# Performance work log

Hardware: AMD Instinct MI355X
Metric: run time of the kernel (lower is better)

Reference implementation:

```python
import jax, jax.numpy as jnp
import numpy as np

DIM = 512
RANK = 256
ORDER = 4
BATCH = 100000
INIT_STD = 0.01


def setup_inputs() -> dict:
    key = jax.random.key(0)
    ks = jax.random.split(key, ORDER + 1)
    inp = {}
    for i in range(ORDER):
        inp[f"f{i}"] = jax.random.normal(ks[i], (DIM, RANK), dtype=jnp.float32) * INIT_STD
    inp["tensor_of_indices"] = jax.random.randint(ks[ORDER], (BATCH, ORDER), 0, DIM, dtype=jnp.int64)
    return inp


def reference(f0, f1, f2, f3, tensor_of_indices):
    # value[b] = sum_r prod_i factors[i][idx[b, i], r]
    # (same math as reconstructing the full CP tensor and gathering entries,
    #  but computed directly per queried index)
    factors = (f0, f1, f2, f3)
    # gather factor rows per mode: each [B, rank]
    prod = factors[0][tensor_of_indices[:, 0]]
    for i in range(1, ORDER):
        prod = prod * factors[i][tensor_of_indices[:, i]]
    return jnp.sum(prod, axis=-1)  # [B]
```

## Files before the change

kernel.cpp:

```cpp
#include <hip/hip_runtime.h>


#define RANK 256

__global__ __launch_bounds__(256) void cp_gather_kernel(
    const float* __restrict__ f0, const float* __restrict__ f1,
    const float* __restrict__ f2, const float* __restrict__ f3,
    const int*   __restrict__ idx,
    float*       __restrict__ out, int batch)
{
    const int wave = (int)((blockIdx.x * blockDim.x + threadIdx.x) >> 6);
    const int lane = (int)(threadIdx.x & 63);
    if (wave >= batch) return;

    const int4 iv = *reinterpret_cast<const int4*>(idx + wave * 4);

    const int r = lane * 4;
    const float4 a = *reinterpret_cast<const float4*>(f0 + (size_t)iv.x * RANK + r);
    const float4 b = *reinterpret_cast<const float4*>(f1 + (size_t)iv.y * RANK + r);
    const float4 c = *reinterpret_cast<const float4*>(f2 + (size_t)iv.z * RANK + r);
    const float4 d = *reinterpret_cast<const float4*>(f3 + (size_t)iv.w * RANK + r);

    float s = a.x * b.x * c.x * d.x
            + a.y * b.y * c.y * d.y
            + a.z * b.z * c.z * d.z
            + a.w * b.w * c.w * d.w;

    #pragma unroll
    for (int off = 32; off > 0; off >>= 1)
        s += __shfl_down(s, off);

    if (lane == 0) out[wave] = s;
}

extern "C" void kernel_launch(void* const* d_in, const int* in_sizes, int n_in,
                              void* d_out, int out_size, void* d_ws, size_t ws_size,
                              hipStream_t stream) {
    const float* f0  = (const float*)d_in[0];
    const float* f1  = (const float*)d_in[1];
    const float* f2  = (const float*)d_in[2];
    const float* f3  = (const float*)d_in[3];
    const int*   idx = (const int*)d_in[4];
    float* out = (float*)d_out;

    const int batch = out_size;
    const int threads = 256;
    const int waves_per_block = threads / 64;
    const int grid = (batch + waves_per_block - 1) / waves_per_block;

    cp_gather_kernel<<<grid, threads, 0, stream>>>(f0, f1, f2, f3, idx, out, batch);
}
```

Measured before the change: 21.72 us.

## Convert factor matrices to fp16 in workspace and gather multiple entries per wave

Adds a pre-pass that converts the four fp32 factor matrices to fp16 in the workspace. A new gather kernel then reads half-width rows and splits each wave into two 32-lane halves, with each wave handling 8 batch entries. The aim is to halve gathered bytes and spread per-wave index-load and reduction overhead over more entries. It adds an extra kernel launch and conversion pass each call, and loses precision by rounding the factors to fp16. An fp32 fallback that processes 4 entries per wave is kept for when the workspace is too small.

After: 20.43 us. 1.06x faster.

```diff
diff --git a/kernel.cpp b/kernel.cpp
--- a/kernel.cpp
+++ b/kernel.cpp
@@ -1,36 +1,134 @@
 #include <hip/hip_runtime.h>
+#include <hip/hip_fp16.h>
 
 
-#define RANK 256
+#define RANK   256
+#define FELEMS (512 * 256)
+#define EPW    8
 
-__global__ __launch_bounds__(256) void cp_gather_kernel(
+__global__ __launch_bounds__(256) void cp_convert_f16(
+    const float* __restrict__ f0, const float* __restrict__ f1,
+    const float* __restrict__ f2, const float* __restrict__ f3,
+    __half* __restrict__ ws)
+{
+    const float* srcs[4] = {f0, f1, f2, f3};
+    const float* __restrict__ src = srcs[blockIdx.y];
+    __half* __restrict__ dst = ws + (size_t)blockIdx.y * FELEMS;
+
+    const int base = (blockIdx.x * 256 + threadIdx.x) * 8;
+    if (base >= FELEMS) return;
+
+    const float4 a = *reinterpret_cast<const float4*>(src + base);
+    const float4 b = *reinterpret_cast<const float4*>(src + base + 4);
+    union { uint4 u; __half2 h[4]; } pk;
+    pk.h[0] = __float22half2_rn(make_float2(a.x, a.y));
+    pk.h[1] = __float22half2_rn(make_float2(a.z, a.w));
+    pk.h[2] = __float22half2_rn(make_float2(b.x, b.y));
+    pk.h[3] = __float22half2_rn(make_float2(b.z, b.w));
+    *reinterpret_cast<uint4*>(dst + base) = pk.u;
+}
+
+__device__ __forceinline__ void cvt8(const uint4 u, float* v) {
+    const __half2* h = reinterpret_cast<const __half2*>(&u);
+    float2 t;
+    t = __half22float2(h[0]); v[0] = t.x; v[1] = t.y;
+    t = __half22float2(h[1]); v[2] = t.x; v[3] = t.y;
+    t = __half22float2(h[2]); v[4] = t.x; v[5] = t.y;
+    t = __half22float2(h[3]); v[6] = t.x; v[7] = t.y;
+}
+
+__global__ __launch_bounds__(256) void cp_gather_f16(
+    const __half* __restrict__ ws, const int* __restrict__ idx,
+    float* __restrict__ out, int batch)
+{
+    const int wid  = (int)((blockIdx.x * blockDim.x + threadIdx.x) >> 6);
+    const int lane = (int)(threadIdx.x & 63);
+    const int e0   = wid * EPW;
+    if (e0 >= batch) return;
+
+    const int half_id = lane >> 5;
+    const int l5      = lane & 31;
+    const int r0      = l5 * 8;
+
+    int  ee[4];
+    int4 iv[4];
+    #pragma unroll
+    for (int p = 0; p < 4; ++p) {
+        ee[p] = e0 + 2 * p + half_id;
+        const int ec = ee[p] < batch ? ee[p] : batch - 1;
+        iv[p] = *reinterpret_cast<const int4*>(idx + (size_t)ec * 4);
+    }
+
+    uint4 raw[4][4];
+    #pragma unroll
+    for (int p = 0; p < 4; ++p) {
+        raw[p][0] = *reinterpret_cast<const uint4*>(ws + 0 * FELEMS + (size_t)iv[p].x * RANK + r0);
+        raw[p][1] = *reinterpret_cast<const uint4*>(ws + 1 * FELEMS + (size_t)iv[p].y * RANK + r0);
+        raw[p][2] = *reinterpret_cast<const uint4*>(ws + 2 * FELEMS + (size_t)iv[p].z * RANK + r0);
+        raw[p][3] = *reinterpret_cast<const uint4*>(ws + 3 * FELEMS + (size_t)iv[p].w * RANK + r0);
+    }
+
+    float s[4];
+    #pragma unroll
+    for (int p = 0; p < 4; ++p) {
+        float va[8], vb[8], vc[8], vd[8];
+        cvt8(raw[p][0], va);
+        cvt8(raw[p][1], vb);
+        cvt8(raw[p][2], vc);
+        cvt8(raw[p][3], vd);
+        float acc = 0.f;
+        #pragma unroll
+        for (int k = 0; k < 8; ++k)
+            acc += va[k] * vb[k] * vc[k] * vd[k];
+        s[p] = acc;
+    }
+
+    #pragma unroll
+    for (int off = 16; off > 0; off >>= 1) {
+        #pragma unroll
+        for (int p = 0; p < 4; ++p)
+            s[p] += __shfl_xor(s[p], off);
+    }
+
+    if (l5 == 0) {
+        #pragma unroll
+        for (int p = 0; p < 4; ++p)
+            if (ee[p] < batch) out[ee[p]] = s[p];
+    }
+}
+
+__global__ __launch_bounds__(256) void cp_gather_f32(
     const float* __restrict__ f0, const float* __restrict__ f1,
     const float* __restrict__ f2, const float* __restrict__ f3,
     const int*   __restrict__ idx,
     float*       __restrict__ out, int batch)
 {
-    const int wave = (int)((blockIdx.x * blockDim.x + threadIdx.x) >> 6);
+    const int wid  = (int)((blockIdx.x * blockDim.x + threadIdx.x) >> 6);
     const int lane = (int)(threadIdx.x & 63);
-    if (wave >= batch) return;
-
-    const int4 iv = *reinterpret_cast<const int4*>(idx + wave * 4);
-
+    const int e0   = wid * 4;
+    if (e0 >= batch) return;
     const int r = lane * 4;
-    const float4 a = *reinterpret_cast<const float4*>(f0 + (size_t)iv.x * RANK + r);
-    const float4 b = *reinterpret_cast<const float4*>(f1 + (size_t)iv.y * RANK + r);
-    const float4 c = *reinterpret_cast<const float4*>(f2 + (size_t)iv.z * RANK + r);
-    const float4 d = *reinterpret_cast<const float4*>(f3 + (size_t)iv.w * RANK + r);
-
-    float s = a.x * b.x * c.x * d.x
-            + a.y * b.y * c.y * d.y
-            + a.z * b.z * c.z * d.z
-            + a.w * b.w * c.w * d.w;
-
+    float s[4];
+    #pragma unroll
+    for (int e = 0; e < 4; ++e) {
+        const int  ec = (e0 + e) < batch ? (e0 + e) : batch - 1;
+        const int4 iv = *reinterpret_cast<const int4*>(idx + (size_t)ec * 4);
+        const float4 a = *reinterpret_cast<const float4*>(f0 + (size_t)iv.x * RANK + r);
+        const float4 b = *reinterpret_cast<const float4*>(f1 + (size_t)iv.y * RANK + r);
+        const float4 c = *reinterpret_cast<const float4*>(f2 + (size_t)iv.z * RANK + r);
+        const float4 d = *reinterpret_cast<const float4*>(f3 + (size_t)iv.w * RANK + r);
+        s[e] = a.x * b.x * c.x * d.x + a.y * b.y * c.y * d.y
+             + a.z * b.z * c.z * d.z + a.w * b.w * c.w * d.w;
+    }
     #pragma unroll
     for (int off = 32; off > 0; off >>= 1)
-        s += __shfl_down(s, off);
-
-    if (lane == 0) out[wave] = s;
+        #pragma unroll
+        for (int e = 0; e < 4; ++e)
+            s[e] += __shfl_xor(s[e], off);
+    if (lane == 0)
+        #pragma unroll
+        for (int e = 0; e < 4; ++e)
+            if (e0 + e < batch) out[e0 + e] = s[e];
 }
 
 extern "C" void kernel_launch(void* const* d_in, const int* in_sizes, int n_in,
@@ -42,11 +140,18 @@
     const float* f3  = (const float*)d_in[3];
     const int*   idx = (const int*)d_in[4];
     float* out = (float*)d_out;
+    const int batch = out_size;
 
-    const int batch = out_size;
-    const int threads = 256;
-    const int waves_per_block = threads / 64;
-    const int grid = (batch + waves_per_block - 1) / waves_per_block;
-
-    cp_gather_kernel<<<grid, threads, 0, stream>>>(f0, f1, f2, f3, idx, out, batch);
+    const size_t ws_needed = (size_t)4 * FELEMS * sizeof(__half);
+    if (ws_size >= ws_needed) {
+        __half* wsf = (__half*)d_ws;
+        dim3 cgrid(FELEMS / (256 * 8), 4);
+        cp_convert_f16<<<cgrid, 256, 0, stream>>>(f0, f1, f2, f3, wsf);
+        const int waves = (batch + EPW - 1) / EPW;
+        const int grid  = (waves + 3) / 4;
+        cp_gather_f16<<<grid, 256, 0, stream>>>(wsf, idx, out, batch);
+    } else {
+        const int grid = (batch + 15) / 16;
+        cp_gather_f32<<<grid, 256, 0, stream>>>(f0, f1, f2, f3, idx, out, batch);
+    }
 }
```

## Stage fp16 rank-sliced factor tiles in LDS with split-rank partial sums

Applied to the files above, without the earlier changes.

Adds a three-kernel path. The first kernel converts the factor matrices to fp16 and lays them out in rank slices of 16. The main kernel then loads one slice of all four factors into 64 KB of swizzled LDS, and each thread computes a partial dot product for its batch elements from that slice. A third kernel sums the 16 partials per element. The aim is to replace scattered global gathers with LDS reads, at the cost of fp16 precision loss, two extra launches and partial-sum traffic through global memory.

Result: slower. 24.45 us (+12.6%).

```diff
diff --git a/kernel.cpp b/kernel.cpp
--- a/kernel.cpp
+++ b/kernel.cpp
@@ -1,36 +1,136 @@
 #include <hip/hip_runtime.h>
+#include <hip/hip_fp16.h>
 
 
-#define RANK 256
+#define DIM    512
+#define RANK   256
+#define W      16
+#define NS     16
+#define NCHUNK 32
+#define FELEMS (DIM * RANK)
 
-__global__ __launch_bounds__(256) void cp_gather_kernel(
+__global__ __launch_bounds__(256) void cp_convert(
+    const float* __restrict__ f0, const float* __restrict__ f1,
+    const float* __restrict__ f2, const float* __restrict__ f3,
+    __half* __restrict__ wsf)
+{
+    const float* srcs[4] = {f0, f1, f2, f3};
+    const int f = blockIdx.y;
+    const int g = blockIdx.x * 256 + threadIdx.x;
+    if (g >= FELEMS / 4) return;
+    const float4 v = *reinterpret_cast<const float4*>(srcs[f] + (size_t)g * 4);
+    const int i = g >> 6;
+    const int s = (g >> 2) & 15;
+    const int r = (g & 3) * 4;
+    union { uint2 u; __half2 h[2]; } pk;
+    pk.h[0] = __float22half2_rn(make_float2(v.x, v.y));
+    pk.h[1] = __float22half2_rn(make_float2(v.z, v.w));
+    *reinterpret_cast<uint2*>(wsf + (((size_t)(s * 4 + f) * DIM + i) * W + r)) = pk.u;
+}
+
+__global__ __launch_bounds__(1024) void cp_main(
+    const __half* __restrict__ wsf, const int* __restrict__ idx,
+    float* __restrict__ partials, int batch)
+{
+    extern __shared__ char smem[];
+    uint2* lds64 = reinterpret_cast<uint2*>(smem);
+
+    const int s     = blockIdx.x & (NS - 1);
+    const int chunk = blockIdx.x >> 4;
+
+    const uint4* src16 = reinterpret_cast<const uint4*>(wsf + (size_t)s * (4 * DIM * W));
+    for (int g = threadIdx.x; g < 4096; g += 1024) {
+        const uint4 v  = src16[g];
+        const int gg   = (g & 1) * 2;
+        const int i    = (g >> 1) & 511;
+        const int f    = g >> 10;
+        const int sw   = (i >> 2) & 3;
+        const int base = f * 2048 + i * 4;
+        lds64[base + (gg ^ sw)]       = make_uint2(v.x, v.y);
+        lds64[base + ((gg + 1) ^ sw)] = make_uint2(v.z, v.w);
+    }
+    __syncthreads();
+
+    const int csz = batch / NCHUNK;
+    const int e0  = chunk * csz;
+    float* pout = partials + (size_t)s * batch;
+    for (int k = threadIdx.x; k < csz; k += 1024) {
+        const int e = e0 + k;
+        const int4 iv = *reinterpret_cast<const int4*>(idx + (size_t)e * 4);
+        const int b0 = iv.x * 4,        sw0 = (iv.x >> 2) & 3;
+        const int b1 = 2048 + iv.y * 4, sw1 = (iv.y >> 2) & 3;
+        const int b2 = 4096 + iv.z * 4, sw2 = (iv.z >> 2) & 3;
+        const int b3 = 6144 + iv.w * 4, sw3 = (iv.w >> 2) & 3;
+        float acc = 0.f;
+        #pragma unroll
+        for (int g = 0; g < 4; ++g) {
+            const uint2 h0 = lds64[b0 + (g ^ sw0)];
+            const uint2 h1 = lds64[b1 + (g ^ sw1)];
+            const uint2 h2 = lds64[b2 + (g ^ sw2)];
+            const uint2 h3 = lds64[b3 + (g ^ sw3)];
+            const __half2* a = reinterpret_cast<const __half2*>(&h0);
+            const __half2* b = reinterpret_cast<const __half2*>(&h1);
+            const __half2* c = reinterpret_cast<const __half2*>(&h2);
+            const __half2* d = reinterpret_cast<const __half2*>(&h3);
+            const float2 a0 = __half22float2(a[0]), a1 = __half22float2(a[1]);
+            const float2 bb0 = __half22float2(b[0]), bb1 = __half22float2(b[1]);
+            const float2 c0 = __half22float2(c[0]), c1 = __half22float2(c[1]);
+            const float2 d0 = __half22float2(d[0]), d1 = __half22float2(d[1]);
+            acc += a0.x * bb0.x * c0.x * d0.x;
+            acc += a0.y * bb0.y * c0.y * d0.y;
+            acc += a1.x * bb1.x * c1.x * d1.x;
+            acc += a1.y * bb1.y * c1.y * d1.y;
+        }
+        pout[e] = acc;
+    }
+}
+
+__global__ __launch_bounds__(256) void cp_reduce(
+    const float* __restrict__ partials, float* __restrict__ out, int batch)
+{
+    const int e = (blockIdx.x * 256 + threadIdx.x) * 4;
+    if (e >= batch) return;
+    float4 acc = make_float4(0.f, 0.f, 0.f, 0.f);
+    #pragma unroll
+    for (int s = 0; s < NS; ++s) {
+        const float4 v = *reinterpret_cast<const float4*>(partials + (size_t)s * batch + e);
+        acc.x += v.x; acc.y += v.y; acc.z += v.z; acc.w += v.w;
+    }
+    *reinterpret_cast<float4*>(out + e) = acc;
+}
+
+__global__ __launch_bounds__(256) void cp_gather_f32(
     const float* __restrict__ f0, const float* __restrict__ f1,
     const float* __restrict__ f2, const float* __restrict__ f3,
     const int*   __restrict__ idx,
     float*       __restrict__ out, int batch)
 {
-    const int wave = (int)((blockIdx.x * blockDim.x + threadIdx.x) >> 6);
+    const int wid  = (int)((blockIdx.x * blockDim.x + threadIdx.x) >> 6);
     const int lane = (int)(threadIdx.x & 63);
-    if (wave >= batch) return;
-
-    const int4 iv = *reinterpret_cast<const int4*>(idx + wave * 4);
-
+    const int e0   = wid * 4;
+    if (e0 >= batch) return;
     const int r = lane * 4;
-    const float4 a = *reinterpret_cast<const float4*>(f0 + (size_t)iv.x * RANK + r);
-    const float4 b = *reinterpret_cast<const float4*>(f1 + (size_t)iv.y * RANK + r);
-    const float4 c = *reinterpret_cast<const float4*>(f2 + (size_t)iv.z * RANK + r);
-    const float4 d = *reinterpret_cast<const float4*>(f3 + (size_t)iv.w * RANK + r);
-
-    float s = a.x * b.x * c.x * d.x
-            + a.y * b.y * c.y * d.y
-            + a.z * b.z * c.z * d.z
-            + a.w * b.w * c.w * d.w;
-
+    float s[4];
+    #pragma unroll
+    for (int e = 0; e < 4; ++e) {
+        const int  ec = (e0 + e) < batch ? (e0 + e) : batch - 1;
+        const int4 iv = *reinterpret_cast<const int4*>(idx + (size_t)ec * 4);
+        const float4 a = *reinterpret_cast<const float4*>(f0 + (size_t)iv.x * RANK + r);
+        const float4 b = *reinterpret_cast<const float4*>(f1 + (size_t)iv.y * RANK + r);
+        const float4 c = *reinterpret_cast<const float4*>(f2 + (size_t)iv.z * RANK + r);
+        const float4 d = *reinterpret_cast<const float4*>(f3 + (size_t)iv.w * RANK + r);
+        s[e] = a.x * b.x * c.x * d.x + a.y * b.y * c.y * d.y
+             + a.z * b.z * c.z * d.z + a.w * b.w * c.w * d.w;
+    }
     #pragma unroll
     for (int off = 32; off > 0; off >>= 1)
-        s += __shfl_down(s, off);
-
-    if (lane == 0) out[wave] = s;
+        #pragma unroll
+        for (int e = 0; e < 4; ++e)
+            s[e] += __shfl_xor(s[e], off);
+    if (lane == 0)
+        #pragma unroll
+        for (int e = 0; e < 4; ++e)
+            if (e0 + e < batch) out[e0 + e] = s[e];
 }
 
 extern "C" void kernel_launch(void* const* d_in, const int* in_sizes, int n_in,
@@ -42,11 +142,19 @@
     const float* f3  = (const float*)d_in[3];
     const int*   idx = (const int*)d_in[4];
     float* out = (float*)d_out;
+    const int batch = out_size;
 
-    const int batch = out_size;
-    const int threads = 256;
-    const int waves_per_block = threads / 64;
-    const int grid = (batch + waves_per_block - 1) / waves_per_block;
+    const size_t f16_bytes = (size_t)4 * FELEMS * sizeof(__half);
+    const size_t ws_needed = f16_bytes + (size_t)NS * batch * sizeof(float);
 
-    cp_gather_kernel<<<grid, threads, 0, stream>>>(f0, f1, f2, f3, idx, out, batch);
+    if (ws_size >= ws_needed && batch % NCHUNK == 0 && batch % 4 == 0) {
+        __half* wsf      = (__half*)d_ws;
+        float*  partials = (float*)((char*)d_ws + f16_bytes);
+        cp_convert<<<dim3(FELEMS / 4 / 256, 4), 256, 0, stream>>>(f0, f1, f2, f3, wsf);
+        cp_main<<<NS * NCHUNK, 1024, 65536, stream>>>(wsf, idx, partials, batch);
+        cp_reduce<<<(batch / 4 + 255) / 256, 256, 0, stream>>>(partials, out, batch);
+    } else {
+        const int grid = (batch + 15) / 16;
+        cp_gather_f32<<<grid, 256, 0, stream>>>(f0, f1, f2, f3, idx, out, batch);
+    }
 }
```

## Split rank into LDS-resident slices with bf16 partials and reduce pass

Applied to the files above, without the earlier changes.

Replaces the per-row global gather with a three-kernel pipeline. The first kernel reshuffles the factors into 16-column rank slices, the second stages each slice of all four factors (128KB) in LDS and gathers from LDS, and the third sums the 16 per-slice partials. The aim is to cut repeated L2/HBM gather traffic by serving factor reads from LDS. In exchange it adds two extra launches, a 16x partial write/read, and stores partials in bf16, which loses precision in the sum. A fallback f32 gather handling four entries per wave is kept.

Result: slower. 23.50 us (+8.2%).

```diff
diff --git a/kernel.cpp b/kernel.cpp
--- a/kernel.cpp
+++ b/kernel.cpp
@@ -1,36 +1,137 @@
 #include <hip/hip_runtime.h>
+#include <hip/hip_bf16.h>
 
 
-#define RANK 256
+#define DIM    512
+#define RANK   256
+#define W      16
+#define NS     16
+#define NCHUNK 16
+#define FELEMS (DIM * RANK)
 
-__global__ __launch_bounds__(256) void cp_gather_kernel(
+typedef float f32x4 __attribute__((ext_vector_type(4)));
+
+__global__ __launch_bounds__(256) void cp_reshuffle(
+    const float* __restrict__ f0, const float* __restrict__ f1,
+    const float* __restrict__ f2, const float* __restrict__ f3,
+    float* __restrict__ wsA)
+{
+    const int g = blockIdx.x * 256 + threadIdx.x;
+    if (g >= NS * 4 * DIM) return;
+    const int i = g & (DIM - 1);
+    const int f = (g >> 9) & 3;
+    const int s = g >> 11;
+    const float* srcs[4] = {f0, f1, f2, f3};
+    const f32x4* src = reinterpret_cast<const f32x4*>(srcs[f] + (size_t)i * RANK + s * W);
+    f32x4* dst = reinterpret_cast<f32x4*>(wsA + (size_t)g * W);
+    dst[0] = src[0]; dst[1] = src[1]; dst[2] = src[2]; dst[3] = src[3];
+}
+
+__global__ __launch_bounds__(1024) void cp_main(
+    const float* __restrict__ wsA, const int* __restrict__ idx,
+    __hip_bfloat16* __restrict__ partials, int batch)
+{
+    extern __shared__ f32x4 lds4[];
+    const int s     = blockIdx.x & (NS - 1);
+    const int chunk = blockIdx.x >> 4;
+
+    const f32x4* src = reinterpret_cast<const f32x4*>(wsA + (size_t)s * (4 * DIM * W));
+    for (int t = threadIdx.x; t < (4 * DIM * W) / 4; t += 1024)
+        lds4[t] = src[t];
+    __syncthreads();
+
+    const int csz  = batch / NCHUNK;
+    const int e0b  = chunk * csz;
+    const int lane = (int)(threadIdx.x & 63);
+    const int wid  = (int)(threadIdx.x >> 6);
+    const int q    = lane & 3;
+    const int eoff = lane >> 2;
+    const int iters = (csz + 255) / 256;
+    const int lim   = batch * 4 - 1;
+
+    __hip_bfloat16* pout = partials + (size_t)s * batch;
+
+    for (int it = 0; it < iters; ++it) {
+        const int e0 = e0b + it * 256 + wid * 16;
+        const int e  = e0 + eoff;
+        const bool valid = (e - e0b) < csz;
+
+        int ia = e0 * 4 + lane;
+        ia = ia < lim ? ia : lim;
+        const int myi = idx[ia];
+
+        const int i0 = __builtin_amdgcn_mov_dpp(myi, 0x00, 0xf, 0xf, true);
+        const int i1 = __builtin_amdgcn_mov_dpp(myi, 0x55, 0xf, 0xf, true);
+        const int i2 = __builtin_amdgcn_mov_dpp(myi, 0xaa, 0xf, 0xf, true);
+        const int i3 = __builtin_amdgcn_mov_dpp(myi, 0xff, 0xf, 0xf, true);
+
+        const f32x4 a = lds4[(0 * DIM + i0) * 4 + q];
+        const f32x4 b = lds4[(1 * DIM + i1) * 4 + q];
+        const f32x4 c = lds4[(2 * DIM + i2) * 4 + q];
+        const f32x4 d = lds4[(3 * DIM + i3) * 4 + q];
+
+        const f32x4 p = a * b * c * d;
+        float sum = (p.x + p.y) + (p.z + p.w);
+
+        sum += __int_as_float(__builtin_amdgcn_mov_dpp(__float_as_int(sum), 0xB1, 0xf, 0xf, true));
+        sum += __int_as_float(__builtin_amdgcn_mov_dpp(__float_as_int(sum), 0x4E, 0xf, 0xf, true));
+
+        if (q == 0 && valid)
+            pout[e] = __float2bfloat16(sum);
+    }
+}
+
+__global__ __launch_bounds__(256) void cp_reduce(
+    const __hip_bfloat16* __restrict__ partials, float* __restrict__ out, int batch)
+{
+    const int e = (blockIdx.x * 256 + threadIdx.x) * 4;
+    if (e >= batch) return;
+    float ax = 0.f, ay = 0.f, az = 0.f, aw = 0.f;
+    #pragma unroll
+    for (int s = 0; s < NS; ++s) {
+        const uint2 u = *reinterpret_cast<const uint2*>(
+            reinterpret_cast<const unsigned short*>(partials) + (size_t)s * batch + e);
+        ax += __uint_as_float(u.x << 16);
+        ay += __uint_as_float(u.x & 0xffff0000u);
+        az += __uint_as_float(u.y << 16);
+        aw += __uint_as_float(u.y & 0xffff0000u);
+    }
+    float4 acc = make_float4(ax, ay, az, aw);
+    *reinterpret_cast<float4*>(out + e) = acc;
+}
+
+__global__ __launch_bounds__(256) void cp_gather_f32(
     const float* __restrict__ f0, const float* __restrict__ f1,
     const float* __restrict__ f2, const float* __restrict__ f3,
     const int*   __restrict__ idx,
     float*       __restrict__ out, int batch)
 {
-    const int wave = (int)((blockIdx.x * blockDim.x + threadIdx.x) >> 6);
+    const int wid  = (int)((blockIdx.x * blockDim.x + threadIdx.x) >> 6);
     const int lane = (int)(threadIdx.x & 63);
-    if (wave >= batch) return;
-
-    const int4 iv = *reinterpret_cast<const int4*>(idx + wave * 4);
-
+    const int e0   = wid * 4;
+    if (e0 >= batch) return;
     const int r = lane * 4;
-    const float4 a = *reinterpret_cast<const float4*>(f0 + (size_t)iv.x * RANK + r);
-    const float4 b = *reinterpret_cast<const float4*>(f1 + (size_t)iv.y * RANK + r);
-    const float4 c = *reinterpret_cast<const float4*>(f2 + (size_t)iv.z * RANK + r);
-    const float4 d = *reinterpret_cast<const float4*>(f3 + (size_t)iv.w * RANK + r);
-
-    float s = a.x * b.x * c.x * d.x
-            + a.y * b.y * c.y * d.y
-            + a.z * b.z * c.z * d.z
-            + a.w * b.w * c.w * d.w;
-
+    float s[4];
+    #pragma unroll
+    for (int e = 0; e < 4; ++e) {
+        const int  ec = (e0 + e) < batch ? (e0 + e) : batch - 1;
+        const int4 iv = *reinterpret_cast<const int4*>(idx + (size_t)ec * 4);
+        const float4 a = *reinterpret_cast<const float4*>(f0 + (size_t)iv.x * RANK + r);
+        const float4 b = *reinterpret_cast<const float4*>(f1 + (size_t)iv.y * RANK + r);
+        const float4 c = *reinterpret_cast<const float4*>(f2 + (size_t)iv.z * RANK + r);
+        const float4 d = *reinterpret_cast<const float4*>(f3 + (size_t)iv.w * RANK + r);
+        s[e] = a.x * b.x * c.x * d.x + a.y * b.y * c.y * d.y
+             + a.z * b.z * c.z * d.z + a.w * b.w * c.w * d.w;
+    }
     #pragma unroll
     for (int off = 32; off > 0; off >>= 1)
-        s += __shfl_down(s, off);
-
-    if (lane == 0) out[wave] = s;
+        #pragma unroll
+        for (int e = 0; e < 4; ++e)
+            s[e] += __shfl_xor(s[e], off);
+    if (lane == 0)
+        #pragma unroll
+        for (int e = 0; e < 4; ++e)
+            if (e0 + e < batch) out[e0 + e] = s[e];
 }
 
 extern "C" void kernel_launch(void* const* d_in, const int* in_sizes, int n_in,
@@ -42,11 +143,29 @@
     const float* f3  = (const float*)d_in[3];
     const int*   idx = (const int*)d_in[4];
     float* out = (float*)d_out;
+    const int batch = out_size;
 
-    const int batch = out_size;
-    const int threads = 256;
-    const int waves_per_block = threads / 64;
-    const int grid = (batch + waves_per_block - 1) / waves_per_block;
+    const size_t wsA_bytes  = (size_t)NS * 4 * DIM * W * sizeof(float);
+    const size_t part_bytes = (size_t)NS * batch * sizeof(__hip_bfloat16);
+    const size_t ws_needed  = wsA_bytes + part_bytes;
+    const int    lds_bytes  = 4 * DIM * W * (int)sizeof(float);
 
-    cp_gather_kernel<<<grid, threads, 0, stream>>>(f0, f1, f2, f3, idx, out, batch);
+    bool main_path = (ws_size >= ws_needed) && (batch % NCHUNK == 0) && (batch % 4 == 0);
+    if (main_path) {
+        hipError_t err = hipFuncSetAttribute(
+            reinterpret_cast<const void*>(&cp_main),
+            hipFuncAttributeMaxDynamicSharedMemorySize, lds_bytes);
+        if (err != hipSuccess) main_path = false;
+    }
+
+    if (main_path) {
+        float*            wsA      = (float*)d_ws;
+        __hip_bfloat16*   partials = (__hip_bfloat16*)((char*)d_ws + wsA_bytes);
+        cp_reshuffle<<<(NS * 4 * DIM + 255) / 256, 256, 0, stream>>>(f0, f1, f2, f3, wsA);
+        cp_main<<<NS * NCHUNK, 1024, lds_bytes, stream>>>(wsA, idx, partials, batch);
+        cp_reduce<<<(batch / 4 + 255) / 256, 256, 0, stream>>>(partials, out, batch);
+    } else {
+        const int grid = (batch + 15) / 16;
+        cp_gather_f32<<<grid, 256, 0, stream>>>(f0, f1, f2, f3, idx, out, batch);
+    }
 }
```
